# Kernel tuning notes

Measured on AMD Instinct MI355X. Metric: run time of the kernel, lower is better.

The kernel has to match this reference:

```python
import math
import jax, jax.numpy as jnp
import numpy as np

B, C, H, W = 64, 32, 224, 224
MINDEV = np.float32(1.0 / math.sqrt(H * W))


def setup_inputs() -> dict:
    key = jax.random.key(0)
    x = jax.random.normal(key, (B, C, H, W), dtype=jnp.float32)
    return {"x": x}


def reference(x):
    # Per-(batch, channel) mean and unbiased std over the HxW slice,
    # matching torch.std's default ddof=1.
    m = jnp.mean(x, axis=(2, 3), keepdims=True)
    s = jnp.std(x, axis=(2, 3), keepdims=True, ddof=1)
    # Cap std away from zero: dev = max(std, 1/sqrt(H*W))
    s = jnp.maximum(s, jnp.asarray(MINDEV, x.dtype))
    return (x - m) / s
```

## Files before the change

kernel.cpp:

```cpp
#include <hip/hip_runtime.h>
#include <math.h>


namespace {
constexpr int kHW      = 224 * 224;
constexpr int kHW4     = kHW / 4;
constexpr int kThreads = 1024;
constexpr int kFullIt  = kHW4 / kThreads;
constexpr int kExtra   = kHW4 - kFullIt * kThreads;
constexpr float kMinDev = 1.0f / 224.0f;
}

__global__ __launch_bounds__(kThreads, 1)
void whiten_fused(const float* __restrict__ x, float* __restrict__ y) {
    const int bc  = blockIdx.x;
    const int tid = threadIdx.x;
    const float4* __restrict__ xs =
        reinterpret_cast<const float4*>(x) + (size_t)bc * kHW4;
    float4* __restrict__ ys =
        reinterpret_cast<float4*>(y) + (size_t)bc * kHW4;

    float4 v[kFullIt];
    float4 ve = make_float4(0.f, 0.f, 0.f, 0.f);
    const bool extra = (tid < kExtra);
#pragma unroll
    for (int i = 0; i < kFullIt; ++i) v[i] = xs[tid + i * kThreads];
    if (extra) ve = xs[kFullIt * kThreads + tid];

    float s = 0.f, ss = 0.f;
#pragma unroll
    for (int i = 0; i < kFullIt; ++i) {
        s += v[i].x + v[i].y + v[i].z + v[i].w;
        ss = fmaf(v[i].x, v[i].x, ss);
        ss = fmaf(v[i].y, v[i].y, ss);
        ss = fmaf(v[i].z, v[i].z, ss);
        ss = fmaf(v[i].w, v[i].w, ss);
    }
    s += ve.x + ve.y + ve.z + ve.w;
    ss = fmaf(ve.x, ve.x, ss);
    ss = fmaf(ve.y, ve.y, ss);
    ss = fmaf(ve.z, ve.z, ss);
    ss = fmaf(ve.w, ve.w, ss);

#pragma unroll
    for (int off = 32; off >= 1; off >>= 1) {
        s  += __shfl_down(s, off, 64);
        ss += __shfl_down(ss, off, 64);
    }

    __shared__ float wred_s[kThreads / 64];
    __shared__ float wred_q[kThreads / 64];
    __shared__ float stats[2];
    const int wid  = tid >> 6;
    const int lane = tid & 63;
    if (lane == 0) { wred_s[wid] = s; wred_q[wid] = ss; }
    __syncthreads();
    if (tid == 0) {
        float S = 0.f, SS = 0.f;
#pragma unroll
        for (int i = 0; i < kThreads / 64; ++i) { S += wred_s[i]; SS += wred_q[i]; }
        const float mean = S * (1.0f / kHW);
        float var = (SS - S * mean) * (1.0f / (kHW - 1));
        var = fmaxf(var, 0.f);
        const float dev = fmaxf(sqrtf(var), kMinDev);
        stats[0] = mean;
        stats[1] = 1.0f / dev;
    }
    __syncthreads();
    const float mean = stats[0];
    const float rcp  = stats[1];

#pragma unroll
    for (int i = 0; i < kFullIt; ++i) {
        float4 o;
        o.x = (v[i].x - mean) * rcp;
        o.y = (v[i].y - mean) * rcp;
        o.z = (v[i].z - mean) * rcp;
        o.w = (v[i].w - mean) * rcp;
        ys[tid + i * kThreads] = o;
    }
    if (extra) {
        float4 o;
        o.x = (ve.x - mean) * rcp;
        o.y = (ve.y - mean) * rcp;
        o.z = (ve.z - mean) * rcp;
        o.w = (ve.w - mean) * rcp;
        ys[kFullIt * kThreads + tid] = o;
    }
}

extern "C" void kernel_launch(void* const* d_in, const int* in_sizes, int n_in,
                              void* d_out, int out_size, void* d_ws, size_t ws_size,
                              hipStream_t stream) {
    (void)in_sizes; (void)n_in; (void)d_ws; (void)ws_size; (void)out_size;
    const float* x = reinterpret_cast<const float*>(d_in[0]);
    float* y = reinterpret_cast<float*>(d_out);
    const int nSlices = 64 * 32;
    whiten_fused<<<nSlices, kThreads, 0, stream>>>(x, y);
}
```

Before: 156.6 us.

## Process eight slices per block with double-buffered register prefetch

Each block now handles eight (batch, channel) slices instead of one, launching 256 blocks in place of 2048. It alternates between two register buffers so the next slice's loads are in flight while the current slice is reduced and written. This aims to hide the load latency that the single-slice version exposed at every barrier. It also swaps the shared stats broadcast for every thread re-reducing the per-wave partials, with a raw s_waitcnt/s_barrier between the partial writes and the reads. The trade-offs are roughly double the register use per thread and one block per CU for the whole run, which could lower memory parallelism or cause spills.

```diff
diff --git a/kernel.cpp b/kernel.cpp
--- a/kernel.cpp
+++ b/kernel.cpp
@@ -3,89 +3,95 @@
 
 
 namespace {
-constexpr int kHW      = 224 * 224;
-constexpr int kHW4     = kHW / 4;
-constexpr int kThreads = 1024;
-constexpr int kFullIt  = kHW4 / kThreads;
-constexpr int kExtra   = kHW4 - kFullIt * kThreads;
+constexpr int kHW       = 224 * 224;
+constexpr int kHW4      = kHW / 4;
+constexpr int kThreads  = 1024;
+constexpr int kIt       = kHW4 / kThreads;
+constexpr int kExtra    = kHW4 - kIt * kThreads;
+constexpr int kSlices   = 64 * 32;
+constexpr int kPerBlock = 8;
+constexpr int kBlocks   = kSlices / kPerBlock;
+constexpr int kWaves    = kThreads / 64;
 constexpr float kMinDev = 1.0f / 224.0f;
 }
 
-__global__ __launch_bounds__(kThreads, 1)
-void whiten_fused(const float* __restrict__ x, float* __restrict__ y) {
-    const int bc  = blockIdx.x;
-    const int tid = threadIdx.x;
-    const float4* __restrict__ xs =
-        reinterpret_cast<const float4*>(x) + (size_t)bc * kHW4;
-    float4* __restrict__ ys =
-        reinterpret_cast<float4*>(y) + (size_t)bc * kHW4;
+__global__ __launch_bounds__(kThreads, 4)
+void whiten_pipe(const float* __restrict__ x, float* __restrict__ y) {
+    __shared__ float2 wred[2][kWaves];
 
-    float4 v[kFullIt];
-    float4 ve = make_float4(0.f, 0.f, 0.f, 0.f);
+    const int  tid   = threadIdx.x;
+    const int  wid   = tid >> 6;
+    const int  lane  = tid & 63;
     const bool extra = (tid < kExtra);
+    const size_t base = (size_t)blockIdx.x * kPerBlock * kHW4;
+    const float4* __restrict__ xs = reinterpret_cast<const float4*>(x) + base;
+    float4* __restrict__ ys       = reinterpret_cast<float4*>(y) + base;
+
+    float4 va[kIt + 1], vb[kIt + 1];
+
+    auto load = [&](float4 (&v)[kIt + 1], int s) {
+        const float4* __restrict__ p = xs + (size_t)s * kHW4;
 #pragma unroll
-    for (int i = 0; i < kFullIt; ++i) v[i] = xs[tid + i * kThreads];
-    if (extra) ve = xs[kFullIt * kThreads + tid];
+        for (int i = 0; i < kIt; ++i) v[i] = p[tid + i * kThreads];
+        if (extra) v[kIt] = p[kIt * kThreads + tid];
+        else       v[kIt] = make_float4(0.f, 0.f, 0.f, 0.f);
+    };
 
-    float s = 0.f, ss = 0.f;
+    auto process = [&](float4 (&v)[kIt + 1], int s, int buf) {
+        float sum = 0.f, ssq = 0.f;
 #pragma unroll
-    for (int i = 0; i < kFullIt; ++i) {
-        s += v[i].x + v[i].y + v[i].z + v[i].w;
-        ss = fmaf(v[i].x, v[i].x, ss);
-        ss = fmaf(v[i].y, v[i].y, ss);
-        ss = fmaf(v[i].z, v[i].z, ss);
-        ss = fmaf(v[i].w, v[i].w, ss);
-    }
-    s += ve.x + ve.y + ve.z + ve.w;
-    ss = fmaf(ve.x, ve.x, ss);
-    ss = fmaf(ve.y, ve.y, ss);
-    ss = fmaf(ve.z, ve.z, ss);
-    ss = fmaf(ve.w, ve.w, ss);
-
+        for (int i = 0; i < kIt + 1; ++i) {
+            sum += v[i].x + v[i].y + v[i].z + v[i].w;
+            ssq = fmaf(v[i].x, v[i].x, ssq);
+            ssq = fmaf(v[i].y, v[i].y, ssq);
+            ssq = fmaf(v[i].z, v[i].z, ssq);
+            ssq = fmaf(v[i].w, v[i].w, ssq);
+        }
 #pragma unroll
-    for (int off = 32; off >= 1; off >>= 1) {
-        s  += __shfl_down(s, off, 64);
-        ss += __shfl_down(ss, off, 64);
-    }
-
-    __shared__ float wred_s[kThreads / 64];
-    __shared__ float wred_q[kThreads / 64];
-    __shared__ float stats[2];
-    const int wid  = tid >> 6;
-    const int lane = tid & 63;
-    if (lane == 0) { wred_s[wid] = s; wred_q[wid] = ss; }
-    __syncthreads();
-    if (tid == 0) {
+        for (int off = 32; off >= 1; off >>= 1) {
+            sum += __shfl_down(sum, off, 64);
+            ssq += __shfl_down(ssq, off, 64);
+        }
+        if (lane == 0) wred[buf][wid] = make_float2(sum, ssq);
+        asm volatile("s_waitcnt lgkmcnt(0)\n\ts_barrier" ::: "memory");
         float S = 0.f, SS = 0.f;
 #pragma unroll
-        for (int i = 0; i < kThreads / 64; ++i) { S += wred_s[i]; SS += wred_q[i]; }
+        for (int i = 0; i < kWaves; ++i) {
+            const float2 t = wred[buf][i];
+            S += t.x; SS += t.y;
+        }
         const float mean = S * (1.0f / kHW);
         float var = (SS - S * mean) * (1.0f / (kHW - 1));
         var = fmaxf(var, 0.f);
-        const float dev = fmaxf(sqrtf(var), kMinDev);
-        stats[0] = mean;
-        stats[1] = 1.0f / dev;
-    }
-    __syncthreads();
-    const float mean = stats[0];
-    const float rcp  = stats[1];
+        const float rcp = 1.0f / fmaxf(sqrtf(var), kMinDev);
 
+        float4* __restrict__ p = ys + (size_t)s * kHW4;
 #pragma unroll
-    for (int i = 0; i < kFullIt; ++i) {
-        float4 o;
-        o.x = (v[i].x - mean) * rcp;
-        o.y = (v[i].y - mean) * rcp;
-        o.z = (v[i].z - mean) * rcp;
-        o.w = (v[i].w - mean) * rcp;
-        ys[tid + i * kThreads] = o;
-    }
-    if (extra) {
-        float4 o;
-        o.x = (ve.x - mean) * rcp;
-        o.y = (ve.y - mean) * rcp;
-        o.z = (ve.z - mean) * rcp;
-        o.w = (ve.w - mean) * rcp;
-        ys[kFullIt * kThreads + tid] = o;
+        for (int i = 0; i < kIt; ++i) {
+            float4 o;
+            o.x = (v[i].x - mean) * rcp;
+            o.y = (v[i].y - mean) * rcp;
+            o.z = (v[i].z - mean) * rcp;
+            o.w = (v[i].w - mean) * rcp;
+            p[tid + i * kThreads] = o;
+        }
+        if (extra) {
+            float4 o;
+            o.x = (v[kIt].x - mean) * rcp;
+            o.y = (v[kIt].y - mean) * rcp;
+            o.z = (v[kIt].z - mean) * rcp;
+            o.w = (v[kIt].w - mean) * rcp;
+            p[kIt * kThreads + tid] = o;
+        }
+    };
+
+    load(va, 0);
+#pragma unroll
+    for (int s = 0; s < kPerBlock; s += 2) {
+        load(vb, s + 1);
+        process(va, s, 0);
+        if (s + 2 < kPerBlock) load(va, s + 2);
+        process(vb, s + 1, 1);
     }
 }
 
@@ -95,6 +101,5 @@
     (void)in_sizes; (void)n_in; (void)d_ws; (void)ws_size; (void)out_size;
     const float* x = reinterpret_cast<const float*>(d_in[0]);
     float* y = reinterpret_cast<float*>(d_out);
-    const int nSlices = 64 * 32;
-    whiten_fused<<<nSlices, kThreads, 0, stream>>>(x, y);
+    whiten_pipe<<<kBlocks, kThreads, 0, stream>>>(x, y);
 }
```

New measurement: 174.5 us. +11.4%, slower.

## Re-read input in second pass instead of holding slice in registers

Applied to the files above, without the earlier changes.

The kernel no longer holds the whole 224x224 slice in registers (12 float4 per thread). It now streams the input twice: once to compute the sum and sum of squares, and again to normalize. Launch bounds are raised to allow far more resident blocks per CU. Outputs are written with nontemporal stores to avoid polluting the cache, so the second read of the slice (about 200KB per block) is more likely to hit L2 or MALL. The cost is extra global read traffic if those re-reads miss the cache.

```diff
diff --git a/kernel.cpp b/kernel.cpp
--- a/kernel.cpp
+++ b/kernel.cpp
@@ -6,86 +6,87 @@
 constexpr int kHW      = 224 * 224;
 constexpr int kHW4     = kHW / 4;
 constexpr int kThreads = 1024;
-constexpr int kFullIt  = kHW4 / kThreads;
-constexpr int kExtra   = kHW4 - kFullIt * kThreads;
+constexpr int kIt      = kHW4 / kThreads;
+constexpr int kExtra   = kHW4 - kIt * kThreads;
+constexpr int kSlices  = 64 * 32;
+constexpr int kWaves   = kThreads / 64;
 constexpr float kMinDev = 1.0f / 224.0f;
+
+typedef float vfloat4 __attribute__((ext_vector_type(4)));
 }
 
-__global__ __launch_bounds__(kThreads, 1)
-void whiten_fused(const float* __restrict__ x, float* __restrict__ y) {
-    const int bc  = blockIdx.x;
-    const int tid = threadIdx.x;
-    const float4* __restrict__ xs =
-        reinterpret_cast<const float4*>(x) + (size_t)bc * kHW4;
-    float4* __restrict__ ys =
-        reinterpret_cast<float4*>(y) + (size_t)bc * kHW4;
+__global__ __launch_bounds__(kThreads, 8)
+void whiten_twopass(const float* __restrict__ x, float* __restrict__ y) {
+    __shared__ float wred_s[kWaves];
+    __shared__ float wred_q[kWaves];
+    __shared__ float stats[2];
 
-    float4 v[kFullIt];
-    float4 ve = make_float4(0.f, 0.f, 0.f, 0.f);
+    const int tid  = threadIdx.x;
+    const int wid  = tid >> 6;
+    const int lane = tid & 63;
     const bool extra = (tid < kExtra);
+    const size_t base = (size_t)blockIdx.x * kHW4;
+    const vfloat4* __restrict__ xs = reinterpret_cast<const vfloat4*>(x) + base;
+    vfloat4* __restrict__ ys       = reinterpret_cast<vfloat4*>(y) + base;
+
+    float sum = 0.f, ssq = 0.f;
 #pragma unroll
-    for (int i = 0; i < kFullIt; ++i) v[i] = xs[tid + i * kThreads];
-    if (extra) ve = xs[kFullIt * kThreads + tid];
-
-    float s = 0.f, ss = 0.f;
-#pragma unroll
-    for (int i = 0; i < kFullIt; ++i) {
-        s += v[i].x + v[i].y + v[i].z + v[i].w;
-        ss = fmaf(v[i].x, v[i].x, ss);
-        ss = fmaf(v[i].y, v[i].y, ss);
-        ss = fmaf(v[i].z, v[i].z, ss);
-        ss = fmaf(v[i].w, v[i].w, ss);
+    for (int i = 0; i < kIt; ++i) {
+        const vfloat4 v = xs[tid + i * kThreads];
+        sum += v.x + v.y + v.z + v.w;
+        ssq = fmaf(v.x, v.x, ssq);
+        ssq = fmaf(v.y, v.y, ssq);
+        ssq = fmaf(v.z, v.z, ssq);
+        ssq = fmaf(v.w, v.w, ssq);
     }
-    s += ve.x + ve.y + ve.z + ve.w;
-    ss = fmaf(ve.x, ve.x, ss);
-    ss = fmaf(ve.y, ve.y, ss);
-    ss = fmaf(ve.z, ve.z, ss);
-    ss = fmaf(ve.w, ve.w, ss);
+    if (extra) {
+        const vfloat4 v = xs[kIt * kThreads + tid];
+        sum += v.x + v.y + v.z + v.w;
+        ssq = fmaf(v.x, v.x, ssq);
+        ssq = fmaf(v.y, v.y, ssq);
+        ssq = fmaf(v.z, v.z, ssq);
+        ssq = fmaf(v.w, v.w, ssq);
+    }
 
 #pragma unroll
     for (int off = 32; off >= 1; off >>= 1) {
-        s  += __shfl_down(s, off, 64);
-        ss += __shfl_down(ss, off, 64);
+        sum += __shfl_down(sum, off, 64);
+        ssq += __shfl_down(ssq, off, 64);
     }
-
-    __shared__ float wred_s[kThreads / 64];
-    __shared__ float wred_q[kThreads / 64];
-    __shared__ float stats[2];
-    const int wid  = tid >> 6;
-    const int lane = tid & 63;
-    if (lane == 0) { wred_s[wid] = s; wred_q[wid] = ss; }
+    if (lane == 0) { wred_s[wid] = sum; wred_q[wid] = ssq; }
     __syncthreads();
     if (tid == 0) {
         float S = 0.f, SS = 0.f;
 #pragma unroll
-        for (int i = 0; i < kThreads / 64; ++i) { S += wred_s[i]; SS += wred_q[i]; }
+        for (int i = 0; i < kWaves; ++i) { S += wred_s[i]; SS += wred_q[i]; }
         const float mean = S * (1.0f / kHW);
         float var = (SS - S * mean) * (1.0f / (kHW - 1));
         var = fmaxf(var, 0.f);
-        const float dev = fmaxf(sqrtf(var), kMinDev);
         stats[0] = mean;
-        stats[1] = 1.0f / dev;
+        stats[1] = 1.0f / fmaxf(sqrtf(var), kMinDev);
     }
     __syncthreads();
     const float mean = stats[0];
     const float rcp  = stats[1];
 
 #pragma unroll
-    for (int i = 0; i < kFullIt; ++i) {
-        float4 o;
-        o.x = (v[i].x - mean) * rcp;
-        o.y = (v[i].y - mean) * rcp;
-        o.z = (v[i].z - mean) * rcp;
-        o.w = (v[i].w - mean) * rcp;
-        ys[tid + i * kThreads] = o;
+    for (int i = 0; i < kIt; ++i) {
+        const vfloat4 v = xs[tid + i * kThreads];
+        vfloat4 o;
+        o.x = (v.x - mean) * rcp;
+        o.y = (v.y - mean) * rcp;
+        o.z = (v.z - mean) * rcp;
+        o.w = (v.w - mean) * rcp;
+        __builtin_nontemporal_store(o, &ys[tid + i * kThreads]);
     }
     if (extra) {
-        float4 o;
-        o.x = (ve.x - mean) * rcp;
-        o.y = (ve.y - mean) * rcp;
-        o.z = (ve.z - mean) * rcp;
-        o.w = (ve.w - mean) * rcp;
-        ys[kFullIt * kThreads + tid] = o;
+        const vfloat4 v = xs[kIt * kThreads + tid];
+        vfloat4 o;
+        o.x = (v.x - mean) * rcp;
+        o.y = (v.y - mean) * rcp;
+        o.z = (v.z - mean) * rcp;
+        o.w = (v.w - mean) * rcp;
+        __builtin_nontemporal_store(o, &ys[kIt * kThreads + tid]);
     }
 }
 
@@ -95,6 +96,5 @@
     (void)in_sizes; (void)n_in; (void)d_ws; (void)ws_size; (void)out_size;
     const float* x = reinterpret_cast<const float*>(d_in[0]);
     float* y = reinterpret_cast<float*>(d_out);
-    const int nSlices = 64 * 32;
-    whiten_fused<<<nSlices, kThreads, 0, stream>>>(x, y);
+    whiten_twopass<<<kSlices, kThreads, 0, stream>>>(x, y);
 }
```

Measured after the change: 175.5 us. +12.1%, slower.
